# Optimization experiments

Measured on AMD Instinct MI355X. Metric: run time of the kernel, lower is better.

## Reference

```python
import jax, jax.numpy as jnp
import numpy as np

B, S, E = 2, 2048, 2048
NH, NKV = 32, 8
HD = E // NH  # 64


def apply_rope(x, cos, sin):
    # x: [B, S, H, D]; cos/sin: [S, D]
    s, d = x.shape[1], x.shape[3]
    c = cos[:s, :d][None, :, None, :]
    sn = sin[:s, :d][None, :, None, :]
    x_rot = jnp.concatenate([-x[..., d // 2:], x[..., : d // 2]], axis=-1)
    return x * c + x_rot * sn


def setup_inputs() -> dict:
    key = jax.random.key(0)
    ks = jax.random.split(key, 6)
    x = jax.random.normal(ks[0], (B, S, E), dtype=jnp.float32)
    mask = jnp.ones((B, S), dtype=bool)
    # RoPE tables [S, HD]
    inv_freq = 1.0 / (10000.0 ** (jnp.arange(0, HD, 2, dtype=jnp.float32) / HD))
    freqs = jnp.arange(S, dtype=jnp.float32)[:, None] * inv_freq[None, :]
    emb = jnp.concatenate([freqs, freqs], axis=-1)  # [S, HD]
    cos = jnp.cos(emb)
    sin = jnp.sin(emb)
    sc = 1.0 / np.sqrt(E)
    Wq = jax.random.normal(ks[1], (E, E), dtype=jnp.float32) * sc
    Wk = jax.random.normal(ks[2], (NKV * HD, E), dtype=jnp.float32) * sc
    Wv = jax.random.normal(ks[3], (NKV * HD, E), dtype=jnp.float32) * sc
    Wo = jax.random.normal(ks[4], (E, E), dtype=jnp.float32) * sc
    return {"x": x, "mask": mask, "cos": cos, "sin": sin,
            "Wq": Wq, "Wk": Wk, "Wv": Wv, "Wo": Wo}


def reference(x, mask, cos, sin, Wq, Wk, Wv, Wo):
    b, s, e = x.shape
    scale = 1.0 / np.sqrt(HD)
    q = (x @ Wq.T).reshape(b, s, NH, HD)
    k = (x @ Wk.T).reshape(b, s, NKV, HD)
    v = (x @ Wv.T).reshape(b, s, NKV, HD)
    q = apply_rope(q, cos, sin)
    k = apply_rope(k, cos, sin)
    rep = NH // NKV
    # expand kv heads: [B,S,NKV,HD] -> [B,S,NH,HD]
    k = jnp.repeat(k, rep, axis=2)
    v = jnp.repeat(v, rep, axis=2)
    # [B,H,S,S]
    scores = jnp.einsum('bqhd,bkhd->bhqk', q, k) * scale
    causal = jnp.tril(jnp.ones((s, s), dtype=bool))
    combined = mask[:, None, None, :] & causal[None, None, :, :]
    scores = jnp.where(combined, scores, -jnp.inf)
    attn = jax.nn.softmax(scores, axis=-1)
    ctx = jnp.einsum('bhqk,bkhd->bqhd', attn, v).reshape(b, s, e)
    return ctx @ Wo.T
```

## Files before the change

kernel.cpp:

```cpp
#include <hip/hip_runtime.h>


typedef __attribute__((ext_vector_type(4))) float f32x4;
typedef __attribute__((ext_vector_type(16))) float f32x16;
typedef __attribute__((ext_vector_type(8))) __bf16 bf16x8;

#define SCL 0.18033688011112042f

__device__ __forceinline__ short f2bf(float f) {
  union { float f; unsigned u; } c; c.f = f;
  unsigned r = c.u + 0x7FFFu + ((c.u >> 16) & 1u);
  return (short)(r >> 16);
}

#define GLOAD16(g, l)                                                      \
  __builtin_amdgcn_global_load_lds(                                        \
      (const __attribute__((address_space(1))) unsigned int*)(g),          \
      (__attribute__((address_space(3))) unsigned int*)(l), 16, 0, 0)

#define VM_WAIT4() asm volatile("s_waitcnt vmcnt(4)" ::: "memory")
#define VM_WAIT0() asm volatile("s_waitcnt vmcnt(0)" ::: "memory")
#define BARRIER()                        \
  do {                                   \
    __builtin_amdgcn_s_barrier();        \
    asm volatile("" ::: "memory");       \
  } while (0)

__device__ __forceinline__ f32x4 mfma16(bf16x8 a, bf16x8 b, f32x4 c) {
  return __builtin_amdgcn_mfma_f32_16x16x32_bf16(a, b, c, 0, 0, 0);
}
__device__ __forceinline__ f32x16 mfma32(bf16x8 a, bf16x8 b, f32x16 c) {
  return __builtin_amdgcn_mfma_f32_32x32x16_bf16(a, b, c, 0, 0, 0);
}

__global__ void conv_bf16(const float* __restrict__ src, short* __restrict__ dst, int n) {
  int i = (blockIdx.x * blockDim.x + threadIdx.x) * 4;
  if (i >= n) return;
  float4 v = *(const float4*)(src + i);
  *(short4*)(dst + i) = make_short4(f2bf(v.x), f2bf(v.y), f2bf(v.z), f2bf(v.w));
}

template <int EPI>
__global__ __launch_bounds__(256, 2)
void gemm_bt(const short* __restrict__ A, const short* __restrict__ B,
             float* __restrict__ C, short* __restrict__ outK,
             short* __restrict__ outV, const float* __restrict__ cosT,
             const float* __restrict__ sinT, int M, int N, int K) {
  __shared__ short As[3][128 * 32];
  __shared__ short Bs[3][128 * 32];
  const int tid = threadIdx.x;
  const int lane = tid & 63;
  const int wm = (tid >> 6) >> 1;
  const int wn = (tid >> 6) & 1;
  const int m0 = blockIdx.x * 128;
  const int n0 = blockIdx.y * 128;
  const int kr = lane >> 4;
  const int lc = lane & 15;

  f32x4 acc[4][4] = {};

  const int lin0 = tid * 16;
  const int row0 = lin0 >> 6;
  const int slot0 = (lin0 >> 4) & 3;
  const int gs0 = slot0 ^ ((row0 >> 1) & 3);
  const int row1 = row0 + 64;
  const int gs1 = slot0 ^ ((row1 >> 1) & 3);
  const short* Ag0 = A + (size_t)(m0 + row0) * K + gs0 * 8;
  const short* Ag1 = A + (size_t)(m0 + row1) * K + gs1 * 8;
  const short* Bg0 = B + (size_t)(n0 + row0) * K + gs0 * 8;
  const short* Bg1 = B + (size_t)(n0 + row1) * K + gs1 * 8;
  const int dA0 = tid * 8;
  const int dA1 = tid * 8 + 2048;

  auto STAGE = [&](int k0, int buf) {
    GLOAD16(Ag0 + k0, &As[buf][dA0]);
    GLOAD16(Ag1 + k0, &As[buf][dA1]);
    GLOAD16(Bg0 + k0, &Bs[buf][dA0]);
    GLOAD16(Bg1 + k0, &Bs[buf][dA1]);
  };

  STAGE(0, 0);
  STAGE(32, 1);
  const int nk = K >> 5;
  for (int ik = 0; ik < nk; ++ik) {
    if (ik + 1 < nk) VM_WAIT4(); else VM_WAIT0();
    BARRIER();
    if (ik + 2 < nk) STAGE((ik + 2) << 5, (ik + 2) % 3);
    const int cur = ik % 3;
    bf16x8 af[4], bfr[4];
#pragma unroll
    for (int i = 0; i < 4; ++i) {
      int r = wm * 64 + i * 16 + lc;
      af[i] = *(const bf16x8*)(&As[cur][r * 32 + ((kr ^ ((r >> 1) & 3)) << 3)]);
    }
#pragma unroll
    for (int j = 0; j < 4; ++j) {
      int r = wn * 64 + j * 16 + lc;
      bfr[j] = *(const bf16x8*)(&Bs[cur][r * 32 + ((kr ^ ((r >> 1) & 3)) << 3)]);
    }
    __builtin_amdgcn_s_setprio(1);
#pragma unroll
    for (int i = 0; i < 4; ++i)
#pragma unroll
      for (int j = 0; j < 4; ++j)
        acc[i][j] = mfma16(af[i], bfr[j], acc[i][j]);
    __builtin_amdgcn_s_setprio(0);
  }

  if constexpr (EPI == 0) {
#pragma unroll
    for (int i = 0; i < 4; ++i) {
      int r0 = m0 + wm * 64 + i * 16 + kr * 4;
#pragma unroll
      for (int j = 0; j < 4; ++j) {
        int c = n0 + wn * 64 + j * 16 + lc;
#pragma unroll
        for (int ii = 0; ii < 4; ++ii)
          C[(size_t)(r0 + ii) * N + c] = acc[i][j][ii];
      }
    }
  } else if constexpr (EPI == 1) {
#pragma unroll
    for (int i = 0; i < 4; ++i) {
#pragma unroll
      for (int ii = 0; ii < 4; ++ii) {
        int r = m0 + wm * 64 + i * 16 + kr * 4 + ii;
        int s = r & 2047;
#pragma unroll
        for (int jp = 0; jp < 2; ++jp) {
          int d = jp * 16 + lc;
          float cs = cosT[s * 64 + d], sn = sinT[s * 64 + d];
          float x0 = acc[i][jp][ii], x1 = acc[i][jp + 2][ii];
          size_t base = (size_t)r * N + n0 + wn * 64;
          outK[base + jp * 16 + lc] = f2bf((x0 * cs - x1 * sn) * SCL);
          outK[base + (jp + 2) * 16 + lc] = f2bf((x1 * cs + x0 * sn) * SCL);
        }
      }
    }
  } else {
    if (n0 < 512) {
#pragma unroll
      for (int i = 0; i < 4; ++i) {
#pragma unroll
        for (int ii = 0; ii < 4; ++ii) {
          int r = m0 + wm * 64 + i * 16 + kr * 4 + ii;
          int s = r & 2047;
#pragma unroll
          for (int jp = 0; jp < 2; ++jp) {
            int d = jp * 16 + lc;
            float cs = cosT[s * 64 + d], sn = sinT[s * 64 + d];
            float x0 = acc[i][jp][ii], x1 = acc[i][jp + 2][ii];
            size_t base = (size_t)r * 512 + n0 + wn * 64;
            outK[base + jp * 16 + lc] = f2bf(x0 * cs - x1 * sn);
            outK[base + (jp + 2) * 16 + lc] = f2bf(x1 * cs + x0 * sn);
          }
        }
      }
    } else {
#pragma unroll
      for (int i = 0; i < 4; ++i) {
#pragma unroll
        for (int ii = 0; ii < 4; ++ii) {
          int r = m0 + wm * 64 + i * 16 + kr * 4 + ii;
#pragma unroll
          for (int j = 0; j < 4; ++j)
            outV[(size_t)r * 512 + (n0 - 512) + wn * 64 + j * 16 + lc] =
                f2bf(acc[i][j][ii]);
        }
      }
    }
  }
}

__global__ void transpose_v(const short* __restrict__ vtmp, short* __restrict__ vt) {
  __shared__ short Ls[64 * 66];
  int s0 = blockIdx.x * 64;
  int h = blockIdx.y;
  int b = blockIdx.z;
  int tid = threadIdx.x;
#pragma unroll
  for (int it = 0; it < 16; ++it) {
    int lin = it * 256 + tid;
    int r = lin >> 6, c = lin & 63;
    Ls[c * 66 + r] = vtmp[(size_t)(b * 2048 + s0 + r) * 512 + h * 64 + c];
  }
  __syncthreads();
#pragma unroll
  for (int it = 0; it < 16; ++it) {
    int lin = it * 256 + tid;
    int d = lin >> 6, c2 = lin & 63;
    vt[((size_t)((b * 8 + h) * 64 + d)) * 2048 + s0 + c2] = Ls[d * 66 + c2];
  }
}

__global__ __launch_bounds__(256, 2)
void attn(const short* __restrict__ Q, const short* __restrict__ Kk,
          const short* __restrict__ Vt, short* __restrict__ O) {
  const int p = blockIdx.x;
  const int h = blockIdx.y;
  const int b = blockIdx.z;
  const int kvh = h >> 2;
  const int tid = threadIdx.x;
  const int lane = tid & 63;
  const int w = tid >> 6;
  const int l5 = lane >> 5;
  const int lc5 = lane & 31;

  __shared__ short Ks[3][4096];
  __shared__ short Vs[3][4096];

  const short* kbs = Kk + (size_t)b * 2048 * 512 + kvh * 64;
  const short* vbs = Vt + (size_t)((b * 8 + kvh) * 64) * 2048;

  const int srow = tid >> 3;
  const int sslot = tid & 7;
  const int gs = sslot ^ (srow & 7);

  auto STAGE = [&](int kt, int buf) {
    const short* kp = kbs + (size_t)(kt * 64 + srow) * 512 + gs * 8;
    GLOAD16(kp, &Ks[buf][tid * 8]);
    GLOAD16(kp + 32 * 512, &Ks[buf][tid * 8 + 2048]);
    const short* vp = vbs + (size_t)srow * 2048 + kt * 64 + gs * 8;
    GLOAD16(vp, &Vs[buf][tid * 8]);
    GLOAD16(vp + 32 * 2048, &Vs[buf][tid * 8 + 2048]);
  };

  const int rx = lc5 & 7;

#pragma unroll 1
  for (int pass = 0; pass < 2; ++pass) {
    const int qb = pass == 0 ? (15 - p) : p;
    const int q0 = qb * 128;
    const int qrow = q0 + w * 32 + lc5;
    const int ktmax = 2 * qb + 1;

    bf16x8 qreg[4];
    const short* qbase = Q + (size_t)(b * 2048 + qrow) * 2048 + h * 64 + l5 * 8;
#pragma unroll
    for (int s = 0; s < 4; ++s) qreg[s] = *(const bf16x8*)(qbase + s * 16);

    f32x16 oa0 = {}, oa1 = {};
    float mrow = -1e30f, lrow = 0.f;

    __syncthreads();
    STAGE(0, 0);
    STAGE(1, 1);

    for (int kt = 0; kt <= ktmax; ++kt) {
      if (kt < ktmax) VM_WAIT4(); else VM_WAIT0();
      BARRIER();
      if (kt + 2 <= ktmax) STAGE(kt + 2, (kt + 2) % 3);
      const int cur = kt % 3;

      if (kt * 64 <= q0 + w * 32 + 31) {
        f32x16 sa0 = {}, sa1 = {};
        __builtin_amdgcn_s_setprio(1);
#pragma unroll
        for (int s = 0; s < 4; ++s) {
          const int so = (((2 * s + l5) ^ rx) << 3);
          bf16x8 k0f = *(const bf16x8*)(&Ks[cur][lc5 * 64 + so]);
          bf16x8 k1f = *(const bf16x8*)(&Ks[cur][(32 + lc5) * 64 + so]);
          sa0 = mfma32(k0f, qreg[s], sa0);
          sa1 = mfma32(k1f, qreg[s], sa1);
        }
        __builtin_amdgcn_s_setprio(0);

        if (kt * 64 + 63 > q0 + w * 32) {
          const int kbase = kt * 64 + 4 * l5;
#pragma unroll
          for (int r = 0; r < 16; ++r) {
            int k = kbase + (r & 3) + 8 * (r >> 2);
            if (k > qrow) sa0[r] = -1e30f;
            if (k + 32 > qrow) sa1[r] = -1e30f;
          }
        }

        float mx = -1e30f;
#pragma unroll
        for (int r = 0; r < 16; ++r) mx = fmaxf(mx, fmaxf(sa0[r], sa1[r]));
        mx = fmaxf(mx, __shfl_xor(mx, 32));
        if (!__all(mx <= mrow + 8.f)) {
          float nm = fmaxf(mrow, mx);
          float rs = exp2f(mrow - nm);
          mrow = nm;
          lrow *= rs;
#pragma unroll
          for (int r = 0; r < 16; ++r) { oa0[r] *= rs; oa1[r] *= rs; }
        }
        float ps = 0.f;
#pragma unroll
        for (int r = 0; r < 16; ++r) {
          float p0 = exp2f(sa0[r] - mrow);
          float p1 = exp2f(sa1[r] - mrow);
          sa0[r] = p0; sa1[r] = p1;
          ps += p0 + p1;
        }
        ps += __shfl_xor(ps, 32);
        lrow += ps;

        unsigned pk0[8], pk1[8];
#pragma unroll
        for (int a = 0; a < 8; ++a) {
          asm("v_cvt_pk_bf16_f32 %0, %1, %2" : "=v"(pk0[a]) : "v"(sa0[2 * a]), "v"(sa0[2 * a + 1]));
          asm("v_cvt_pk_bf16_f32 %0, %1, %2" : "=v"(pk1[a]) : "v"(sa1[2 * a]), "v"(sa1[2 * a + 1]));
        }

        __builtin_amdgcn_s_setprio(1);
#pragma unroll
        for (int s = 0; s < 4; ++s) {
          const int c = s & 1;
          unsigned x0 = (s < 2) ? pk0[4 * c + 0] : pk1[4 * c + 0];
          unsigned y0 = (s < 2) ? pk0[4 * c + 2] : pk1[4 * c + 2];
          unsigned x1 = (s < 2) ? pk0[4 * c + 1] : pk1[4 * c + 1];
          unsigned y1 = (s < 2) ? pk0[4 * c + 3] : pk1[4 * c + 3];
          asm("v_permlane32_swap_b32 %0, %1" : "+v"(x0), "+v"(y0));
          asm("v_permlane32_swap_b32 %0, %1" : "+v"(x1), "+v"(y1));
          union { unsigned u[4]; bf16x8 v; } pf;
          pf.u[0] = x0; pf.u[1] = x1; pf.u[2] = y0; pf.u[3] = y1;
          const int so = (((2 * s + l5) ^ rx) << 3);
          bf16x8 v0 = *(const bf16x8*)(&Vs[cur][lc5 * 64 + so]);
          bf16x8 v1 = *(const bf16x8*)(&Vs[cur][(32 + lc5) * 64 + so]);
          oa0 = mfma32(v0, pf.v, oa0);
          oa1 = mfma32(v1, pf.v, oa1);
        }
        __builtin_amdgcn_s_setprio(0);
      }
    }

    float inv = 1.0f / lrow;
    short* ob = O + (size_t)(b * 2048 + qrow) * 2048 + h * 64 + 4 * l5;
#pragma unroll
    for (int g = 0; g < 4; ++g) {
      *(short4*)(ob + 8 * g) =
          make_short4(f2bf(oa0[4 * g + 0] * inv), f2bf(oa0[4 * g + 1] * inv),
                      f2bf(oa0[4 * g + 2] * inv), f2bf(oa0[4 * g + 3] * inv));
      *(short4*)(ob + 32 + 8 * g) =
          make_short4(f2bf(oa1[4 * g + 0] * inv), f2bf(oa1[4 * g + 1] * inv),
                      f2bf(oa1[4 * g + 2] * inv), f2bf(oa1[4 * g + 3] * inv));
    }
  }
}

extern "C" void kernel_launch(void* const* d_in, const int* in_sizes, int n_in,
                              void* d_out, int out_size, void* d_ws, size_t ws_size,
                              hipStream_t stream) {
  (void)in_sizes; (void)n_in; (void)out_size; (void)ws_size;
  const float* x    = (const float*)d_in[0];
  const float* cosT = (const float*)d_in[2];
  const float* sinT = (const float*)d_in[3];
  const float* Wq   = (const float*)d_in[4];
  const float* Wk   = (const float*)d_in[5];
  const float* Wv   = (const float*)d_in[6];
  const float* Wo   = (const float*)d_in[7];

  char* ws = (char*)d_ws;
  short* xb   = (short*)(ws + 0);
  short* Wqob = (short*)(ws + 16777216);
  short* Wkvb = (short*)(ws + 25165824);
  short* qr   = (short*)(ws + 29360128);
  short* kb   = (short*)(ws + 46137344);
  short* vtmp = (short*)(ws + 50331648);
  short* vt   = (short*)(ws + 54525952);
  short* ctx  = (short*)(ws + 58720256);

  conv_bf16<<<8192, 256, 0, stream>>>(x, xb, 8388608);
  conv_bf16<<<4096, 256, 0, stream>>>(Wq, Wqob, 4194304);
  conv_bf16<<<1024, 256, 0, stream>>>(Wk, Wkvb, 1048576);
  conv_bf16<<<1024, 256, 0, stream>>>(Wv, Wkvb + 1048576, 1048576);

  gemm_bt<1><<<dim3(32, 16), 256, 0, stream>>>(xb, Wqob, nullptr, qr, nullptr,
                                               cosT, sinT, 4096, 2048, 2048);
  gemm_bt<2><<<dim3(32, 8), 256, 0, stream>>>(xb, Wkvb, nullptr, kb, vtmp,
                                              cosT, sinT, 4096, 1024, 2048);

  transpose_v<<<dim3(32, 8, 2), 256, 0, stream>>>(vtmp, vt);
  conv_bf16<<<4096, 256, 0, stream>>>(Wo, Wqob, 4194304);

  attn<<<dim3(8, 32, 2), 256, 0, stream>>>(qr, kb, vt, ctx);

  gemm_bt<0><<<dim3(32, 16), 256, 0, stream>>>(ctx, Wqob, (float*)d_out, nullptr,
                                               nullptr, nullptr, nullptr,
                                               4096, 2048, 2048);
}
```

Baseline: 343.9 us.

## Rewrite GEMMs as 256x128 MFMA32 tiles and fuse Q/KV projections

Replaces the 128x128 GEMM (256 threads, 16x16x32 MFMA, BK=32) with a 256x128 tile kernel using 512 threads, 32x32x16 MFMA, BK=64, triple-buffered dynamic LDS and an XCD-aware block swizzle. The Q and KV projections become one launch over N=3072, relying on the Q and KV weights sitting next to each other in the workspace. A per-column epilogue then routes each tile to the Q, K or V output, applying RoPE where needed. The aim is more data reuse per LDS load, fewer launches and better L2 locality. The cost is higher LDS and register use per block, which may lower occupancy.

```diff
diff --git a/kernel.cpp b/kernel.cpp
--- a/kernel.cpp
+++ b/kernel.cpp
@@ -18,6 +18,7 @@
       (const __attribute__((address_space(1))) unsigned int*)(g),          \
       (__attribute__((address_space(3))) unsigned int*)(l), 16, 0, 0)
 
+#define VM_WAIT6() asm volatile("s_waitcnt vmcnt(6)" ::: "memory")
 #define VM_WAIT4() asm volatile("s_waitcnt vmcnt(4)" ::: "memory")
 #define VM_WAIT0() asm volatile("s_waitcnt vmcnt(0)" ::: "memory")
 #define BARRIER()                        \
@@ -26,9 +27,6 @@
     asm volatile("" ::: "memory");       \
   } while (0)
 
-__device__ __forceinline__ f32x4 mfma16(bf16x8 a, bf16x8 b, f32x4 c) {
-  return __builtin_amdgcn_mfma_f32_16x16x32_bf16(a, b, c, 0, 0, 0);
-}
 __device__ __forceinline__ f32x16 mfma32(bf16x8 a, bf16x8 b, f32x16 c) {
   return __builtin_amdgcn_mfma_f32_32x32x16_bf16(a, b, c, 0, 0, 0);
 }
@@ -41,131 +39,117 @@
 }
 
 template <int EPI>
-__global__ __launch_bounds__(256, 2)
-void gemm_bt(const short* __restrict__ A, const short* __restrict__ B,
-             float* __restrict__ C, short* __restrict__ outK,
-             short* __restrict__ outV, const float* __restrict__ cosT,
-             const float* __restrict__ sinT, int M, int N, int K) {
-  __shared__ short As[3][128 * 32];
-  __shared__ short Bs[3][128 * 32];
+__global__ __launch_bounds__(512)
+void gemm256(const short* __restrict__ A, const short* __restrict__ B,
+             float* __restrict__ C, short* __restrict__ outQ,
+             short* __restrict__ outK, short* __restrict__ outV,
+             const float* __restrict__ cosT, const float* __restrict__ sinT,
+             int M, int N, int K) {
+  extern __shared__ short lds[];
+  short* Asb = lds;
+  short* Bsb = lds + 3 * 16384;
   const int tid = threadIdx.x;
   const int lane = tid & 63;
-  const int wm = (tid >> 6) >> 1;
-  const int wn = (tid >> 6) & 1;
-  const int m0 = blockIdx.x * 128;
-  const int n0 = blockIdx.y * 128;
-  const int kr = lane >> 4;
-  const int lc = lane & 15;
-
-  f32x4 acc[4][4] = {};
-
-  const int lin0 = tid * 16;
-  const int row0 = lin0 >> 6;
-  const int slot0 = (lin0 >> 4) & 3;
-  const int gs0 = slot0 ^ ((row0 >> 1) & 3);
-  const int row1 = row0 + 64;
-  const int gs1 = slot0 ^ ((row1 >> 1) & 3);
-  const short* Ag0 = A + (size_t)(m0 + row0) * K + gs0 * 8;
-  const short* Ag1 = A + (size_t)(m0 + row1) * K + gs1 * 8;
-  const short* Bg0 = B + (size_t)(n0 + row0) * K + gs0 * 8;
-  const short* Bg1 = B + (size_t)(n0 + row1) * K + gs1 * 8;
-  const int dA0 = tid * 8;
-  const int dA1 = tid * 8 + 2048;
+  const int wid = tid >> 6;
+  const int wm = wid >> 1;
+  const int wn = wid & 1;
+  const int l5 = lane >> 5, lc5 = lane & 31;
+
+  const int nwg = gridDim.x;
+  const int cpx = nwg >> 3;
+  const int swz = ((int)blockIdx.x & 7) * cpx + ((int)blockIdx.x >> 3);
+  const int MT = M >> 8;
+  const int mt = swz % MT, nt = swz / MT;
+  const int m0 = mt << 8, n0 = nt << 7;
+
+  const int srow = tid >> 3;
+  const int gsl = (tid & 7) ^ (srow & 7);
+  const short* Ag = A + (size_t)(m0 + srow) * K + gsl * 8;
+  const short* Bg = B + (size_t)(n0 + srow) * K + gsl * 8;
 
   auto STAGE = [&](int k0, int buf) {
-    GLOAD16(Ag0 + k0, &As[buf][dA0]);
-    GLOAD16(Ag1 + k0, &As[buf][dA1]);
-    GLOAD16(Bg0 + k0, &Bs[buf][dA0]);
-    GLOAD16(Bg1 + k0, &Bs[buf][dA1]);
+    short* ad = Asb + buf * 16384 + tid * 8;
+    const short* ag = Ag + k0;
+#pragma unroll
+    for (int p = 0; p < 4; ++p)
+      GLOAD16(ag + (size_t)(p * 64) * K, ad + p * 4096);
+    short* bd = Bsb + buf * 8192 + tid * 8;
+    const short* bg = Bg + k0;
+#pragma unroll
+    for (int p = 0; p < 2; ++p)
+      GLOAD16(bg + (size_t)(p * 64) * K, bd + p * 4096);
   };
 
+  f32x16 acc[2][2] = {};
+
   STAGE(0, 0);
-  STAGE(32, 1);
-  const int nk = K >> 5;
-  for (int ik = 0; ik < nk; ++ik) {
-    if (ik + 1 < nk) VM_WAIT4(); else VM_WAIT0();
+  STAGE(64, 1);
+  const int nk = K >> 6;
+  for (int t = 0; t < nk; ++t) {
+    if (t + 1 < nk) VM_WAIT6(); else VM_WAIT0();
     BARRIER();
-    if (ik + 2 < nk) STAGE((ik + 2) << 5, (ik + 2) % 3);
-    const int cur = ik % 3;
-    bf16x8 af[4], bfr[4];
-#pragma unroll
-    for (int i = 0; i < 4; ++i) {
-      int r = wm * 64 + i * 16 + lc;
-      af[i] = *(const bf16x8*)(&As[cur][r * 32 + ((kr ^ ((r >> 1) & 3)) << 3)]);
-    }
-#pragma unroll
-    for (int j = 0; j < 4; ++j) {
-      int r = wn * 64 + j * 16 + lc;
-      bfr[j] = *(const bf16x8*)(&Bs[cur][r * 32 + ((kr ^ ((r >> 1) & 3)) << 3)]);
-    }
-    __builtin_amdgcn_s_setprio(1);
-#pragma unroll
-    for (int i = 0; i < 4; ++i)
-#pragma unroll
-      for (int j = 0; j < 4; ++j)
-        acc[i][j] = mfma16(af[i], bfr[j], acc[i][j]);
-    __builtin_amdgcn_s_setprio(0);
+    if (t + 2 < nk) STAGE((t + 2) << 6, (t + 2) % 3);
+    const short* Ab = Asb + (t % 3) * 16384;
+    const short* Bb = Bsb + (t % 3) * 8192;
+
+    bf16x8 bfr[2][4];
+#pragma unroll
+    for (int ni = 0; ni < 2; ++ni) {
+      const int row = (2 * wn + ni) * 32 + lc5;
+#pragma unroll
+      for (int s = 0; s < 4; ++s)
+        bfr[ni][s] = *(const bf16x8*)(Bb + row * 64 + (((2 * s + l5) ^ (row & 7)) << 3));
+    }
+#pragma unroll
+    for (int mi = 0; mi < 2; ++mi) {
+      const int row = (2 * wm + mi) * 32 + lc5;
+      bf16x8 af[4];
+#pragma unroll
+      for (int s = 0; s < 4; ++s)
+        af[s] = *(const bf16x8*)(Ab + row * 64 + (((2 * s + l5) ^ (row & 7)) << 3));
+      __builtin_amdgcn_s_setprio(1);
+#pragma unroll
+      for (int s = 0; s < 4; ++s) {
+        acc[mi][0] = mfma32(af[s], bfr[0][s], acc[mi][0]);
+        acc[mi][1] = mfma32(af[s], bfr[1][s], acc[mi][1]);
+      }
+      __builtin_amdgcn_s_setprio(0);
+    }
   }
 
   if constexpr (EPI == 0) {
 #pragma unroll
-    for (int i = 0; i < 4; ++i) {
-      int r0 = m0 + wm * 64 + i * 16 + kr * 4;
-#pragma unroll
-      for (int j = 0; j < 4; ++j) {
-        int c = n0 + wn * 64 + j * 16 + lc;
-#pragma unroll
-        for (int ii = 0; ii < 4; ++ii)
-          C[(size_t)(r0 + ii) * N + c] = acc[i][j][ii];
+    for (int mi = 0; mi < 2; ++mi) {
+      const int rb = m0 + (2 * wm + mi) * 32 + 4 * l5;
+#pragma unroll
+      for (int ni = 0; ni < 2; ++ni) {
+        const int c = n0 + (2 * wn + ni) * 32 + lc5;
+#pragma unroll
+        for (int r = 0; r < 16; ++r)
+          C[(size_t)(rb + (r & 3) + 8 * (r >> 2)) * N + c] = acc[mi][ni][r];
       }
     }
-  } else if constexpr (EPI == 1) {
-#pragma unroll
-    for (int i = 0; i < 4; ++i) {
-#pragma unroll
-      for (int ii = 0; ii < 4; ++ii) {
-        int r = m0 + wm * 64 + i * 16 + kr * 4 + ii;
-        int s = r & 2047;
-#pragma unroll
-        for (int jp = 0; jp < 2; ++jp) {
-          int d = jp * 16 + lc;
-          float cs = cosT[s * 64 + d], sn = sinT[s * 64 + d];
-          float x0 = acc[i][jp][ii], x1 = acc[i][jp + 2][ii];
-          size_t base = (size_t)r * N + n0 + wn * 64;
-          outK[base + jp * 16 + lc] = f2bf((x0 * cs - x1 * sn) * SCL);
-          outK[base + (jp + 2) * 16 + lc] = f2bf((x1 * cs + x0 * sn) * SCL);
-        }
-      }
-    }
   } else {
-    if (n0 < 512) {
-#pragma unroll
-      for (int i = 0; i < 4; ++i) {
-#pragma unroll
-        for (int ii = 0; ii < 4; ++ii) {
-          int r = m0 + wm * 64 + i * 16 + kr * 4 + ii;
-          int s = r & 2047;
-#pragma unroll
-          for (int jp = 0; jp < 2; ++jp) {
-            int d = jp * 16 + lc;
-            float cs = cosT[s * 64 + d], sn = sinT[s * 64 + d];
-            float x0 = acc[i][jp][ii], x1 = acc[i][jp + 2][ii];
-            size_t base = (size_t)r * 512 + n0 + wn * 64;
-            outK[base + jp * 16 + lc] = f2bf(x0 * cs - x1 * sn);
-            outK[base + (jp + 2) * 16 + lc] = f2bf(x1 * cs + x0 * sn);
-          }
-        }
-      }
-    } else {
-#pragma unroll
-      for (int i = 0; i < 4; ++i) {
-#pragma unroll
-        for (int ii = 0; ii < 4; ++ii) {
-          int r = m0 + wm * 64 + i * 16 + kr * 4 + ii;
-#pragma unroll
-          for (int j = 0; j < 4; ++j)
-            outV[(size_t)r * 512 + (n0 - 512) + wn * 64 + j * 16 + lc] =
-                f2bf(acc[i][j][ii]);
+    const int c0 = n0 + wn * 64 + lc5;
+#pragma unroll
+    for (int mi = 0; mi < 2; ++mi) {
+      const int rb = m0 + (2 * wm + mi) * 32 + 4 * l5;
+#pragma unroll
+      for (int r = 0; r < 16; ++r) {
+        const int row = rb + (r & 3) + 8 * (r >> 2);
+        const int s = row & 2047;
+        const float x0 = acc[mi][0][r], x1 = acc[mi][1][r];
+        if (c0 < 2048) {
+          const float cs = cosT[s * 64 + lc5], sn = sinT[s * 64 + lc5];
+          outQ[(size_t)row * 2048 + c0] = f2bf((x0 * cs - x1 * sn) * SCL);
+          outQ[(size_t)row * 2048 + c0 + 32] = f2bf((x1 * cs + x0 * sn) * SCL);
+        } else if (c0 < 2560) {
+          const float cs = cosT[s * 64 + lc5], sn = sinT[s * 64 + lc5];
+          outK[(size_t)row * 512 + (c0 - 2048)] = f2bf(x0 * cs - x1 * sn);
+          outK[(size_t)row * 512 + (c0 - 2048) + 32] = f2bf(x1 * cs + x0 * sn);
+        } else {
+          outV[(size_t)row * 512 + (c0 - 2560)] = f2bf(x0);
+          outV[(size_t)row * 512 + (c0 - 2560) + 32] = f2bf(x1);
         }
       }
     }
@@ -363,22 +347,28 @@
   short* vt   = (short*)(ws + 54525952);
   short* ctx  = (short*)(ws + 58720256);
 
+  const int LDSB = 3 * (16384 + 8192) * 2;
+  {
+    auto* f0 = gemm256<0>;
+    auto* f1 = gemm256<1>;
+    hipFuncSetAttribute((const void*)f0, hipFuncAttributeMaxDynamicSharedMemorySize, LDSB);
+    hipFuncSetAttribute((const void*)f1, hipFuncAttributeMaxDynamicSharedMemorySize, LDSB);
+  }
+
   conv_bf16<<<8192, 256, 0, stream>>>(x, xb, 8388608);
   conv_bf16<<<4096, 256, 0, stream>>>(Wq, Wqob, 4194304);
   conv_bf16<<<1024, 256, 0, stream>>>(Wk, Wkvb, 1048576);
   conv_bf16<<<1024, 256, 0, stream>>>(Wv, Wkvb + 1048576, 1048576);
 
-  gemm_bt<1><<<dim3(32, 16), 256, 0, stream>>>(xb, Wqob, nullptr, qr, nullptr,
-                                               cosT, sinT, 4096, 2048, 2048);
-  gemm_bt<2><<<dim3(32, 8), 256, 0, stream>>>(xb, Wkvb, nullptr, kb, vtmp,
-                                              cosT, sinT, 4096, 1024, 2048);
+  gemm256<1><<<16 * 24, 512, LDSB, stream>>>(xb, Wqob, nullptr, qr, kb, vtmp,
+                                             cosT, sinT, 4096, 3072, 2048);
 
   transpose_v<<<dim3(32, 8, 2), 256, 0, stream>>>(vtmp, vt);
   conv_bf16<<<4096, 256, 0, stream>>>(Wo, Wqob, 4194304);
 
   attn<<<dim3(8, 32, 2), 256, 0, stream>>>(qr, kb, vt, ctx);
 
-  gemm_bt<0><<<dim3(32, 16), 256, 0, stream>>>(ctx, Wqob, (float*)d_out, nullptr,
-                                               nullptr, nullptr, nullptr,
-                                               4096, 2048, 2048);
-}
+  gemm256<0><<<16 * 16, 512, LDSB, stream>>>(ctx, Wqob, (float*)d_out, nullptr,
+                                             nullptr, nullptr, nullptr, nullptr,
+                                             4096, 2048, 2048);
+}
```

Result: no change. 349.6 us (+1.7%).
